# Kernel tuning notes

Measured on AMD Instinct MI355X. Metric: run time of the kernel, lower is better.

Reference implementation:

```python
import jax, jax.numpy as jnp
import numpy as np

S, N, H, E, L = 2048, 32, 512, 256, 2


def setup_inputs() -> dict:
    key = jax.random.key(0)
    ks = jax.random.split(key, 16)
    s = 0.05  # weight scale for stability
    return {
        "x": jax.random.randint(ks[0], (N,), 0, 10),
        "encoder_states": jax.random.normal(ks[1], (S, N, 2 * H), jnp.float32),
        "hidden": jax.random.normal(ks[2], (L, N, H), jnp.float32),
        "cell": jax.random.normal(ks[3], (L, N, H), jnp.float32),
        "W_energy": jax.random.normal(ks[4], (1, 3 * H), jnp.float32) * s,
        "b_energy": jnp.zeros((1,), jnp.float32),
        "emb_table": jax.random.normal(ks[5], (10, E), jnp.float32),
        "wih0": jax.random.normal(ks[6], (4 * H, 2 * H + E), jnp.float32) * s,
        "whh0": jax.random.normal(ks[7], (4 * H, H), jnp.float32) * s,
        "bih0": jnp.zeros((4 * H,), jnp.float32),
        "bhh0": jnp.zeros((4 * H,), jnp.float32),
        "wih1": jax.random.normal(ks[8], (4 * H, H), jnp.float32) * s,
        "whh1": jax.random.normal(ks[9], (4 * H, H), jnp.float32) * s,
        "bih1": jnp.zeros((4 * H,), jnp.float32),
        "bhh1": jnp.zeros((4 * H,), jnp.float32),
        "Wc": jax.random.normal(ks[10], (10, H), jnp.float32) * s,
        "bc": jnp.zeros((10,), jnp.float32),
    }


def _lstm_cell(x, h, c, wih, whh, bih, bhh):
    # PyTorch gate order: i, f, g, o
    gates = x @ wih.T + bih + h @ whh.T + bhh  # [N, 4H]
    i, f, g, o = jnp.split(gates, 4, axis=-1)
    c_new = jax.nn.sigmoid(f) * c + jax.nn.sigmoid(i) * jnp.tanh(g)
    h_new = jax.nn.sigmoid(o) * jnp.tanh(c_new)
    return h_new, c_new


def reference(x, encoder_states, hidden, cell, W_energy, b_energy, emb_table,
              wih0, whh0, bih0, bhh0, wih1, whh1, bih1, bhh1, Wc, bc):
    seq_len = encoder_states.shape[0]
    h_last = hidden[-1]  # [N, H]
    h_rep = jnp.broadcast_to(h_last, (seq_len,) + h_last.shape)  # [S, N, H]
    cat = jnp.concatenate([h_rep, encoder_states], axis=2)  # [S, N, 3H]
    energy = jax.nn.relu(cat @ W_energy.T + b_energy)  # [S, N, 1]
    attn = jax.nn.softmax(energy, axis=0)  # softmax over seq dim
    context = jnp.einsum('snk,snl->knl', attn, encoder_states)  # [1, N, 2H]
    emb = emb_table[x][None]  # [1, N, E]
    inp = jnp.concatenate([context, emb], axis=2)[0]  # [N, 2H+E]
    h0, c0 = _lstm_cell(inp, hidden[0], cell[0], wih0, whh0, bih0, bhh0)
    h1, c1 = _lstm_cell(h0, hidden[1], cell[1], wih1, whh1, bih1, bhh1)
    predictions = h1 @ Wc.T + bc  # [N, 10]
    hidden_new = jnp.stack([h0, h1], axis=0)
    cell_new = jnp.stack([c0, c1], axis=0)
    return predictions, hidden_new, cell_new
```

## Files before the change

### kernel.cpp

```cpp
#include <hip/hip_runtime.h>

#define SS 2048
#define NN_ 32
#define HH 512
#define EE 256
#define TWO_H 1024

#define OUT_PRED 0
#define OUT_H0 320
#define OUT_H1 16704
#define OUT_C0 33088
#define OUT_C1 49472

#define WS_ACC 0
#define WS_SUMW 1048576
#define WS_XCAT0 1049600
#define WS_PG0 0
#define WS_XCAT1 262144
#define WS_PG1 294912

__device__ __forceinline__ float wave_reduce(float v) {
  v += __shfl_xor(v, 32);
  v += __shfl_xor(v, 16);
  v += __shfl_xor(v, 8);
  v += __shfl_xor(v, 4);
  v += __shfl_xor(v, 2);
  v += __shfl_xor(v, 1);
  return v;
}

__device__ __forceinline__ float sigmoidf_(float x) { return 1.0f / (1.0f + __expf(-x)); }

__global__ __launch_bounds__(256, 4) void attn_pass(
    const float* __restrict__ enc, const float* __restrict__ hidden,
    const float* __restrict__ We, const float* __restrict__ be,
    float* __restrict__ ws) {
  const int blk = blockIdx.x;
  const int n = blk >> 5;
  const int chunk = blk & 31;
  const int t = threadIdx.x;
  const int wave = t >> 6;
  const int lane = t & 63;

  const float* hl = hidden + (size_t)(NN_ + n) * HH;
  float cp;
  {
    float4 a = *(const float4*)(hl + lane * 8);
    float4 b = *(const float4*)(hl + lane * 8 + 4);
    float4 wa = *(const float4*)(We + lane * 8);
    float4 wb = *(const float4*)(We + lane * 8 + 4);
    cp = a.x * wa.x + a.y * wa.y + a.z * wa.z + a.w * wa.w +
         b.x * wb.x + b.y * wb.y + b.z * wb.z + b.w * wb.w;
  }
  cp = wave_reduce(cp);
  const float c_n = cp + be[0];

  const float4 w0 = *(const float4*)(We + HH + 0 * 256 + lane * 4);
  const float4 w1 = *(const float4*)(We + HH + 1 * 256 + lane * 4);
  const float4 w2 = *(const float4*)(We + HH + 2 * 256 + lane * 4);
  const float4 w3 = *(const float4*)(We + HH + 3 * 256 + lane * 4);

  float4 acc0 = {0, 0, 0, 0}, acc1 = {0, 0, 0, 0}, acc2 = {0, 0, 0, 0}, acc3 = {0, 0, 0, 0};
  float sumw = 0.f;

  const int sBase = chunk * 64 + wave * 16;
#pragma unroll 2
  for (int i = 0; i < 16; ++i) {
    const float* row = enc + ((size_t)(sBase + i) * NN_ + n) * TWO_H;
    float4 e0 = *(const float4*)(row + 0 * 256 + lane * 4);
    float4 e1 = *(const float4*)(row + 1 * 256 + lane * 4);
    float4 e2 = *(const float4*)(row + 2 * 256 + lane * 4);
    float4 e3 = *(const float4*)(row + 3 * 256 + lane * 4);
    float d = e0.x * w0.x + e0.y * w0.y + e0.z * w0.z + e0.w * w0.w +
              e1.x * w1.x + e1.y * w1.y + e1.z * w1.z + e1.w * w1.w +
              e2.x * w2.x + e2.y * w2.y + e2.z * w2.z + e2.w * w2.w +
              e3.x * w3.x + e3.y * w3.y + e3.z * w3.z + e3.w * w3.w;
    d = wave_reduce(d);
    float en = c_n + d;
    en = en > 0.f ? en : 0.f;
    float p = __expf(en - 4.0f);
    sumw += p;
    acc0.x = fmaf(p, e0.x, acc0.x); acc0.y = fmaf(p, e0.y, acc0.y);
    acc0.z = fmaf(p, e0.z, acc0.z); acc0.w = fmaf(p, e0.w, acc0.w);
    acc1.x = fmaf(p, e1.x, acc1.x); acc1.y = fmaf(p, e1.y, acc1.y);
    acc1.z = fmaf(p, e1.z, acc1.z); acc1.w = fmaf(p, e1.w, acc1.w);
    acc2.x = fmaf(p, e2.x, acc2.x); acc2.y = fmaf(p, e2.y, acc2.y);
    acc2.z = fmaf(p, e2.z, acc2.z); acc2.w = fmaf(p, e2.w, acc2.w);
    acc3.x = fmaf(p, e3.x, acc3.x); acc3.y = fmaf(p, e3.y, acc3.y);
    acc3.z = fmaf(p, e3.z, acc3.z); acc3.w = fmaf(p, e3.w, acc3.w);
  }

  __shared__ __align__(16) float lacc[4][1024];
  __shared__ float lsum[4];
  *(float4*)&lacc[wave][0 * 256 + lane * 4] = acc0;
  *(float4*)&lacc[wave][1 * 256 + lane * 4] = acc1;
  *(float4*)&lacc[wave][2 * 256 + lane * 4] = acc2;
  *(float4*)&lacc[wave][3 * 256 + lane * 4] = acc3;
  if (lane == 0) lsum[wave] = sumw;
  __syncthreads();

  const int j = t * 4;
  float4 o;
  o.x = lacc[0][j + 0] + lacc[1][j + 0] + lacc[2][j + 0] + lacc[3][j + 0];
  o.y = lacc[0][j + 1] + lacc[1][j + 1] + lacc[2][j + 1] + lacc[3][j + 1];
  o.z = lacc[0][j + 2] + lacc[1][j + 2] + lacc[2][j + 2] + lacc[3][j + 2];
  o.w = lacc[0][j + 3] + lacc[1][j + 3] + lacc[2][j + 3] + lacc[3][j + 3];
  *(float4*)&ws[WS_ACC + (size_t)blk * 1024 + j] = o;
  if (t == 0) ws[WS_SUMW + blk] = lsum[0] + lsum[1] + lsum[2] + lsum[3];
}

__global__ __launch_bounds__(256) void reduce_ctx(
    const int* __restrict__ x, const float* __restrict__ emb,
    const float* __restrict__ hidden, float* ws) {
  const int n = blockIdx.x;
  const int t = threadIdx.x;
  float sumw = 0.f;
#pragma unroll
  for (int c = 0; c < 32; ++c) sumw += ws[WS_SUMW + n * 32 + c];
  const float inv = 1.0f / sumw;
  float4 v = {0, 0, 0, 0};
#pragma unroll 4
  for (int c = 0; c < 32; ++c) {
    float4 a = *(const float4*)&ws[WS_ACC + (size_t)(n * 32 + c) * 1024 + t * 4];
    v.x += a.x; v.y += a.y; v.z += a.z; v.w += a.w;
  }
  const int j = t * 4;
  ws[WS_XCAT0 + (j + 0) * NN_ + n] = v.x * inv;
  ws[WS_XCAT0 + (j + 1) * NN_ + n] = v.y * inv;
  ws[WS_XCAT0 + (j + 2) * NN_ + n] = v.z * inv;
  ws[WS_XCAT0 + (j + 3) * NN_ + n] = v.w * inv;
  if (t < 64) {
    const int e0 = t * 4;
    const int xi = x[n];
#pragma unroll
    for (int q = 0; q < 4; ++q)
      ws[WS_XCAT0 + (1024 + e0 + q) * NN_ + n] = emb[xi * EE + e0 + q];
  }
  if (t < 128) {
    const int k0 = t * 4;
#pragma unroll
    for (int q = 0; q < 4; ++q)
      ws[WS_XCAT0 + (1280 + k0 + q) * NN_ + n] = hidden[(size_t)n * HH + k0 + q];
  }
}

__global__ __launch_bounds__(256) void gates0_kernel(
    const float* __restrict__ wih0, const float* __restrict__ whh0, float* __restrict__ ws) {
  __shared__ __align__(16) float xs[448 * 32];
  const int bid = blockIdx.x;
  const int chunk = bid & 3;
  const int hg = bid >> 2;
  const int t = threadIdx.x;
  const int nn = t & 31;
  const int rl = t >> 5;
  const int h = hg * 8 + rl;

  const int kb = chunk * 448;
  const int ke = kb + 448;

  const float* src = ws + WS_XCAT0 + (size_t)kb * 32;
  for (int i = t * 4; i < 448 * 32; i += 1024)
    *(float4*)&xs[i] = *(const float4*)&src[i];
  __syncthreads();

  float a0 = 0.f, a1 = 0.f, a2 = 0.f, a3 = 0.f;

  {
    const int s0e = ke < 1280 ? ke : 1280;
    if (kb < s0e) {
      const float* p0 = wih0 + (size_t)(0 * 512 + h) * 1280 + kb;
      const float* p1 = wih0 + (size_t)(1 * 512 + h) * 1280 + kb;
      const float* p2 = wih0 + (size_t)(2 * 512 + h) * 1280 + kb;
      const float* p3 = wih0 + (size_t)(3 * 512 + h) * 1280 + kb;
      const int len = s0e - kb;
#pragma unroll 2
      for (int k = 0; k < len; k += 4) {
        const float4 w0 = *(const float4*)(p0 + k);
        const float4 w1 = *(const float4*)(p1 + k);
        const float4 w2 = *(const float4*)(p2 + k);
        const float4 w3 = *(const float4*)(p3 + k);
        const float x0 = xs[(k + 0) * 32 + nn];
        const float x1 = xs[(k + 1) * 32 + nn];
        const float x2 = xs[(k + 2) * 32 + nn];
        const float x3 = xs[(k + 3) * 32 + nn];
        a0 += w0.x * x0 + w0.y * x1 + w0.z * x2 + w0.w * x3;
        a1 += w1.x * x0 + w1.y * x1 + w1.z * x2 + w1.w * x3;
        a2 += w2.x * x0 + w2.y * x1 + w2.z * x2 + w2.w * x3;
        a3 += w3.x * x0 + w3.y * x1 + w3.z * x2 + w3.w * x3;
      }
    }
  }
  {
    const int s1b = kb > 1280 ? kb : 1280;
    if (s1b < ke) {
      const int xoff = s1b - kb;
      const float* q0 = whh0 + (size_t)(0 * 512 + h) * 512 + (s1b - 1280);
      const float* q1 = whh0 + (size_t)(1 * 512 + h) * 512 + (s1b - 1280);
      const float* q2 = whh0 + (size_t)(2 * 512 + h) * 512 + (s1b - 1280);
      const float* q3 = whh0 + (size_t)(3 * 512 + h) * 512 + (s1b - 1280);
      const int len = ke - s1b;
#pragma unroll 2
      for (int k = 0; k < len; k += 4) {
        const float4 w0 = *(const float4*)(q0 + k);
        const float4 w1 = *(const float4*)(q1 + k);
        const float4 w2 = *(const float4*)(q2 + k);
        const float4 w3 = *(const float4*)(q3 + k);
        const float x0 = xs[(k + xoff + 0) * 32 + nn];
        const float x1 = xs[(k + xoff + 1) * 32 + nn];
        const float x2 = xs[(k + xoff + 2) * 32 + nn];
        const float x3 = xs[(k + xoff + 3) * 32 + nn];
        a0 += w0.x * x0 + w0.y * x1 + w0.z * x2 + w0.w * x3;
        a1 += w1.x * x0 + w1.y * x1 + w1.z * x2 + w1.w * x3;
        a2 += w2.x * x0 + w2.y * x1 + w2.z * x2 + w2.w * x3;
        a3 += w3.x * x0 + w3.y * x1 + w3.z * x2 + w3.w * x3;
      }
    }
  }

  float* dst = ws + WS_PG0 + ((size_t)chunk * 2048 + h) * 32 + nn;
  dst[0 * 512 * 32] = a0;
  dst[1 * 512 * 32] = a1;
  dst[2 * 512 * 32] = a2;
  dst[3 * 512 * 32] = a3;
}

__global__ __launch_bounds__(256) void lstm0_kernel(
    const float* __restrict__ cell, const float* __restrict__ hidden,
    const float* __restrict__ bih0, const float* __restrict__ bhh0,
    float* __restrict__ out, float* __restrict__ ws) {
  const int g = blockIdx.x * 256 + threadIdx.x;
  const int nn = g & 31;
  const int h = g >> 5;
  float gi = bih0[h] + bhh0[h];
  float gf = bih0[512 + h] + bhh0[512 + h];
  float gg = bih0[1024 + h] + bhh0[1024 + h];
  float go = bih0[1536 + h] + bhh0[1536 + h];
#pragma unroll
  for (int c = 0; c < 4; ++c) {
    const float* p = ws + WS_PG0 + (size_t)c * 2048 * 32;
    gi += p[(0 * 512 + h) * 32 + nn];
    gf += p[(1 * 512 + h) * 32 + nn];
    gg += p[(2 * 512 + h) * 32 + nn];
    go += p[(3 * 512 + h) * 32 + nn];
  }
  const float cprev = cell[(size_t)nn * HH + h];
  const float c0 = sigmoidf_(gf) * cprev + sigmoidf_(gi) * tanhf(gg);
  const float h0 = sigmoidf_(go) * tanhf(c0);
  out[OUT_H0 + nn * HH + h] = h0;
  out[OUT_C0 + nn * HH + h] = c0;
  ws[WS_XCAT1 + h * 32 + nn] = h0;
  ws[WS_XCAT1 + (512 + h) * 32 + nn] = hidden[(size_t)(NN_ + nn) * HH + h];
}

__global__ __launch_bounds__(256) void gates1_kernel(
    const float* __restrict__ wih1, const float* __restrict__ whh1, float* __restrict__ ws) {
  __shared__ __align__(16) float xs[256 * 32];
  const int bid = blockIdx.x;
  const int chunk = bid & 3;
  const int hg = bid >> 2;
  const int t = threadIdx.x;
  const int nn = t & 31;
  const int rl = t >> 5;
  const int h = hg * 8 + rl;
  const int kb = chunk * 256;

  const float* src = ws + WS_XCAT1 + (size_t)kb * 32;
  for (int i = t * 4; i < 256 * 32; i += 1024)
    *(float4*)&xs[i] = *(const float4*)&src[i];
  __syncthreads();

  const float* base = (chunk < 2) ? wih1 : whh1;
  const int koff = (chunk < 2) ? kb : kb - 512;
  const float* p0 = base + (size_t)(0 * 512 + h) * 512 + koff;
  const float* p1 = base + (size_t)(1 * 512 + h) * 512 + koff;
  const float* p2 = base + (size_t)(2 * 512 + h) * 512 + koff;
  const float* p3 = base + (size_t)(3 * 512 + h) * 512 + koff;

  float a0 = 0.f, a1 = 0.f, a2 = 0.f, a3 = 0.f;
#pragma unroll 2
  for (int k = 0; k < 256; k += 4) {
    const float4 w0 = *(const float4*)(p0 + k);
    const float4 w1 = *(const float4*)(p1 + k);
    const float4 w2 = *(const float4*)(p2 + k);
    const float4 w3 = *(const float4*)(p3 + k);
    const float x0 = xs[(k + 0) * 32 + nn];
    const float x1 = xs[(k + 1) * 32 + nn];
    const float x2 = xs[(k + 2) * 32 + nn];
    const float x3 = xs[(k + 3) * 32 + nn];
    a0 += w0.x * x0 + w0.y * x1 + w0.z * x2 + w0.w * x3;
    a1 += w1.x * x0 + w1.y * x1 + w1.z * x2 + w1.w * x3;
    a2 += w2.x * x0 + w2.y * x1 + w2.z * x2 + w2.w * x3;
    a3 += w3.x * x0 + w3.y * x1 + w3.z * x2 + w3.w * x3;
  }

  float* dst = ws + WS_PG1 + ((size_t)chunk * 2048 + h) * 32 + nn;
  dst[0 * 512 * 32] = a0;
  dst[1 * 512 * 32] = a1;
  dst[2 * 512 * 32] = a2;
  dst[3 * 512 * 32] = a3;
}

__global__ __launch_bounds__(256) void lstm1_kernel(
    const float* __restrict__ cell,
    const float* __restrict__ bih1, const float* __restrict__ bhh1,
    float* __restrict__ out, float* __restrict__ ws) {
  const int g = blockIdx.x * 256 + threadIdx.x;
  const int nn = g & 31;
  const int h = g >> 5;
  float gi = bih1[h] + bhh1[h];
  float gf = bih1[512 + h] + bhh1[512 + h];
  float gg = bih1[1024 + h] + bhh1[1024 + h];
  float go = bih1[1536 + h] + bhh1[1536 + h];
#pragma unroll
  for (int c = 0; c < 4; ++c) {
    const float* p = ws + WS_PG1 + (size_t)c * 2048 * 32;
    gi += p[(0 * 512 + h) * 32 + nn];
    gf += p[(1 * 512 + h) * 32 + nn];
    gg += p[(2 * 512 + h) * 32 + nn];
    go += p[(3 * 512 + h) * 32 + nn];
  }
  const float cprev = cell[(size_t)(NN_ + nn) * HH + h];
  const float c1 = sigmoidf_(gf) * cprev + sigmoidf_(gi) * tanhf(gg);
  const float h1 = sigmoidf_(go) * tanhf(c1);
  out[OUT_H1 + nn * HH + h] = h1;
  out[OUT_C1 + nn * HH + h] = c1;
}

__global__ __launch_bounds__(256) void pred_kernel(
    const float* __restrict__ Wc, const float* __restrict__ bc, float* out) {
  const int wid = blockIdx.x * 4 + (threadIdx.x >> 6);
  const int lane = threadIdx.x & 63;
  const int nn = wid / 10;
  const int c = wid % 10;
  const float* hp = out + OUT_H1 + (size_t)nn * HH;
  const float* wp = Wc + (size_t)c * HH;
  float p = 0.f;
#pragma unroll
  for (int j = 0; j < 8; ++j) p += hp[lane * 8 + j] * wp[lane * 8 + j];
  p = wave_reduce(p);
  if (lane == 0) out[OUT_PRED + nn * 10 + c] = p + bc[c];
}

extern "C" void kernel_launch(void* const* d_in, const int* in_sizes, int n_in,
                              void* d_out, int out_size, void* d_ws, size_t ws_size,
                              hipStream_t stream) {
  const int* x = (const int*)d_in[0];
  const float* enc = (const float*)d_in[1];
  const float* hidden = (const float*)d_in[2];
  const float* cell = (const float*)d_in[3];
  const float* We = (const float*)d_in[4];
  const float* be = (const float*)d_in[5];
  const float* emb = (const float*)d_in[6];
  const float* wih0 = (const float*)d_in[7];
  const float* whh0 = (const float*)d_in[8];
  const float* bih0 = (const float*)d_in[9];
  const float* bhh0 = (const float*)d_in[10];
  const float* wih1 = (const float*)d_in[11];
  const float* whh1 = (const float*)d_in[12];
  const float* bih1 = (const float*)d_in[13];
  const float* bhh1 = (const float*)d_in[14];
  const float* Wc = (const float*)d_in[15];
  const float* bc = (const float*)d_in[16];
  float* out = (float*)d_out;
  float* ws = (float*)d_ws;

  hipLaunchKernelGGL(attn_pass, dim3(1024), dim3(256), 0, stream, enc, hidden, We, be, ws);
  hipLaunchKernelGGL(reduce_ctx, dim3(32), dim3(256), 0, stream, x, emb, hidden, ws);
  hipLaunchKernelGGL(gates0_kernel, dim3(256), dim3(256), 0, stream, wih0, whh0, ws);
  hipLaunchKernelGGL(lstm0_kernel, dim3(64), dim3(256), 0, stream, cell, hidden, bih0, bhh0, out, ws);
  hipLaunchKernelGGL(gates1_kernel, dim3(256), dim3(256), 0, stream, wih1, whh1, ws);
  hipLaunchKernelGGL(lstm1_kernel, dim3(64), dim3(256), 0, stream, cell, bih1, bhh1, out, ws);
  hipLaunchKernelGGL(pred_kernel, dim3(80), dim3(256), 0, stream, Wc, bc, out);
}
```

Baseline: 98.12 us.

## Stage LSTM gate weights in shared memory and split K across more blocks

The gate GEMV kernels now load each block's weight tile into padded shared memory with coalesced float4 loads, replacing the strided per-thread global reads. K is split into more chunks (7 for layer 0, 8 for layer 1), so more blocks run, and the LSTM epilogues sum more partials. reduce_ctx is also spread over 256 blocks so the context reduction uses more parallelism. This costs more shared memory per block, more partial-sum traffic, and workspace offsets moved to fit the larger partial buffers.

```diff
diff --git a/kernel.cpp b/kernel.cpp
--- a/kernel.cpp
+++ b/kernel.cpp
@@ -16,8 +16,8 @@
 #define WS_SUMW 1048576
 #define WS_XCAT0 1049600
 #define WS_PG0 0
-#define WS_XCAT1 262144
-#define WS_PG1 294912
+#define WS_XCAT1 458752
+#define WS_PG1 491520
 
 __device__ __forceinline__ float wave_reduce(float v) {
   v += __shfl_xor(v, 32);
@@ -111,112 +111,87 @@
 
 __global__ __launch_bounds__(256) void reduce_ctx(
     const int* __restrict__ x, const float* __restrict__ emb,
-    const float* __restrict__ hidden, float* ws) {
-  const int n = blockIdx.x;
+    const float* __restrict__ hidden, float* __restrict__ ws) {
+  const int b = blockIdx.x;
+  const int n = b >> 3;
+  const int jg = b & 7;
   const int t = threadIdx.x;
-  float sumw = 0.f;
-#pragma unroll
-  for (int c = 0; c < 32; ++c) sumw += ws[WS_SUMW + n * 32 + c];
-  const float inv = 1.0f / sumw;
-  float4 v = {0, 0, 0, 0};
-#pragma unroll 4
-  for (int c = 0; c < 32; ++c) {
-    float4 a = *(const float4*)&ws[WS_ACC + (size_t)(n * 32 + c) * 1024 + t * 4];
-    v.x += a.x; v.y += a.y; v.z += a.z; v.w += a.w;
-  }
-  const int j = t * 4;
-  ws[WS_XCAT0 + (j + 0) * NN_ + n] = v.x * inv;
-  ws[WS_XCAT0 + (j + 1) * NN_ + n] = v.y * inv;
-  ws[WS_XCAT0 + (j + 2) * NN_ + n] = v.z * inv;
-  ws[WS_XCAT0 + (j + 3) * NN_ + n] = v.w * inv;
-  if (t < 64) {
-    const int e0 = t * 4;
-    const int xi = x[n];
-#pragma unroll
-    for (int q = 0; q < 4; ++q)
-      ws[WS_XCAT0 + (1024 + e0 + q) * NN_ + n] = emb[xi * EE + e0 + q];
-  }
   if (t < 128) {
-    const int k0 = t * 4;
-#pragma unroll
-    for (int q = 0; q < 4; ++q)
-      ws[WS_XCAT0 + (1280 + k0 + q) * NN_ + n] = hidden[(size_t)n * HH + k0 + q];
-  }
-}
-
-__global__ __launch_bounds__(256) void gates0_kernel(
+    const int j = jg * 128 + t;
+    float sumw = 0.f;
+#pragma unroll
+    for (int c = 0; c < 32; ++c) sumw += ws[WS_SUMW + n * 32 + c];
+    const float inv = 1.0f / sumw;
+    float v = 0.f;
+#pragma unroll 8
+    for (int c = 0; c < 32; ++c) v += ws[WS_ACC + (size_t)(n * 32 + c) * 1024 + j];
+    ws[WS_XCAT0 + j * NN_ + n] = v * inv;
+  } else if (t < 224) {
+    const int row = jg * 96 + (t - 128);
+    float v;
+    if (row < 256) {
+      v = emb[(size_t)x[n] * EE + row];
+    } else {
+      v = hidden[(size_t)n * HH + (row - 256)];
+    }
+    ws[WS_XCAT0 + (1024 + row) * NN_ + n] = v;
+  }
+}
+
+__global__ __launch_bounds__(256, 2) void gates0_kernel(
     const float* __restrict__ wih0, const float* __restrict__ whh0, float* __restrict__ ws) {
-  __shared__ __align__(16) float xs[448 * 32];
+  __shared__ __align__(16) float xs[256 * 32];
+  __shared__ __align__(16) float wt[32 * 260];
   const int bid = blockIdx.x;
-  const int chunk = bid & 3;
-  const int hg = bid >> 2;
+  const int chunk = bid % 7;
+  const int hg = bid / 7;
   const int t = threadIdx.x;
   const int nn = t & 31;
   const int rl = t >> 5;
+
+  {
+    const float* src = ws + WS_XCAT0 + (size_t)chunk * 256 * 32;
+#pragma unroll
+    for (int i = t * 4; i < 8192; i += 1024)
+      *(float4*)&xs[i] = *(const float4*)&src[i];
+  }
+  {
+    const int r = t >> 3;
+    const int k8 = t & 7;
+    const int grow = (r >> 3) * 512 + hg * 8 + (r & 7);
+    const float* src = (chunk < 5) ? (wih0 + (size_t)grow * 1280 + chunk * 256)
+                                   : (whh0 + (size_t)grow * 512 + (chunk - 5) * 256);
+#pragma unroll
+    for (int jj = 0; jj < 8; ++jj) {
+      const int kl = jj * 32 + k8 * 4;
+      *(float4*)&wt[r * 260 + kl] = *(const float4*)(src + kl);
+    }
+  }
+  __syncthreads();
+
+  const float* w0p = &wt[(0 * 8 + rl) * 260];
+  const float* w1p = &wt[(1 * 8 + rl) * 260];
+  const float* w2p = &wt[(2 * 8 + rl) * 260];
+  const float* w3p = &wt[(3 * 8 + rl) * 260];
+
+  float a0 = 0.f, a1 = 0.f, a2 = 0.f, a3 = 0.f;
+#pragma unroll 4
+  for (int k = 0; k < 256; k += 4) {
+    const float4 w0 = *(const float4*)(w0p + k);
+    const float4 w1 = *(const float4*)(w1p + k);
+    const float4 w2 = *(const float4*)(w2p + k);
+    const float4 w3 = *(const float4*)(w3p + k);
+    const float x0 = xs[(k + 0) * 32 + nn];
+    const float x1 = xs[(k + 1) * 32 + nn];
+    const float x2 = xs[(k + 2) * 32 + nn];
+    const float x3 = xs[(k + 3) * 32 + nn];
+    a0 += w0.x * x0 + w0.y * x1 + w0.z * x2 + w0.w * x3;
+    a1 += w1.x * x0 + w1.y * x1 + w1.z * x2 + w1.w * x3;
+    a2 += w2.x * x0 + w2.y * x1 + w2.z * x2 + w2.w * x3;
+    a3 += w3.x * x0 + w3.y * x1 + w3.z * x2 + w3.w * x3;
+  }
+
   const int h = hg * 8 + rl;
-
-  const int kb = chunk * 448;
-  const int ke = kb + 448;
-
-  const float* src = ws + WS_XCAT0 + (size_t)kb * 32;
-  for (int i = t * 4; i < 448 * 32; i += 1024)
-    *(float4*)&xs[i] = *(const float4*)&src[i];
-  __syncthreads();
-
-  float a0 = 0.f, a1 = 0.f, a2 = 0.f, a3 = 0.f;
-
-  {
-    const int s0e = ke < 1280 ? ke : 1280;
-    if (kb < s0e) {
-      const float* p0 = wih0 + (size_t)(0 * 512 + h) * 1280 + kb;
-      const float* p1 = wih0 + (size_t)(1 * 512 + h) * 1280 + kb;
-      const float* p2 = wih0 + (size_t)(2 * 512 + h) * 1280 + kb;
-      const float* p3 = wih0 + (size_t)(3 * 512 + h) * 1280 + kb;
-      const int len = s0e - kb;
-#pragma unroll 2
-      for (int k = 0; k < len; k += 4) {
-        const float4 w0 = *(const float4*)(p0 + k);
-        const float4 w1 = *(const float4*)(p1 + k);
-        const float4 w2 = *(const float4*)(p2 + k);
-        const float4 w3 = *(const float4*)(p3 + k);
-        const float x0 = xs[(k + 0) * 32 + nn];
-        const float x1 = xs[(k + 1) * 32 + nn];
-        const float x2 = xs[(k + 2) * 32 + nn];
-        const float x3 = xs[(k + 3) * 32 + nn];
-        a0 += w0.x * x0 + w0.y * x1 + w0.z * x2 + w0.w * x3;
-        a1 += w1.x * x0 + w1.y * x1 + w1.z * x2 + w1.w * x3;
-        a2 += w2.x * x0 + w2.y * x1 + w2.z * x2 + w2.w * x3;
-        a3 += w3.x * x0 + w3.y * x1 + w3.z * x2 + w3.w * x3;
-      }
-    }
-  }
-  {
-    const int s1b = kb > 1280 ? kb : 1280;
-    if (s1b < ke) {
-      const int xoff = s1b - kb;
-      const float* q0 = whh0 + (size_t)(0 * 512 + h) * 512 + (s1b - 1280);
-      const float* q1 = whh0 + (size_t)(1 * 512 + h) * 512 + (s1b - 1280);
-      const float* q2 = whh0 + (size_t)(2 * 512 + h) * 512 + (s1b - 1280);
-      const float* q3 = whh0 + (size_t)(3 * 512 + h) * 512 + (s1b - 1280);
-      const int len = ke - s1b;
-#pragma unroll 2
-      for (int k = 0; k < len; k += 4) {
-        const float4 w0 = *(const float4*)(q0 + k);
-        const float4 w1 = *(const float4*)(q1 + k);
-        const float4 w2 = *(const float4*)(q2 + k);
-        const float4 w3 = *(const float4*)(q3 + k);
-        const float x0 = xs[(k + xoff + 0) * 32 + nn];
-        const float x1 = xs[(k + xoff + 1) * 32 + nn];
-        const float x2 = xs[(k + xoff + 2) * 32 + nn];
-        const float x3 = xs[(k + xoff + 3) * 32 + nn];
-        a0 += w0.x * x0 + w0.y * x1 + w0.z * x2 + w0.w * x3;
-        a1 += w1.x * x0 + w1.y * x1 + w1.z * x2 + w1.w * x3;
-        a2 += w2.x * x0 + w2.y * x1 + w2.z * x2 + w2.w * x3;
-        a3 += w3.x * x0 + w3.y * x1 + w3.z * x2 + w3.w * x3;
-      }
-    }
-  }
-
   float* dst = ws + WS_PG0 + ((size_t)chunk * 2048 + h) * 32 + nn;
   dst[0 * 512 * 32] = a0;
   dst[1 * 512 * 32] = a1;
@@ -236,7 +211,7 @@
   float gg = bih0[1024 + h] + bhh0[1024 + h];
   float go = bih0[1536 + h] + bhh0[1536 + h];
 #pragma unroll
-  for (int c = 0; c < 4; ++c) {
+  for (int c = 0; c < 7; ++c) {
     const float* p = ws + WS_PG0 + (size_t)c * 2048 * 32;
     gi += p[(0 * 512 + h) * 32 + nn];
     gf += p[(1 * 512 + h) * 32 + nn];
@@ -252,37 +227,50 @@
   ws[WS_XCAT1 + (512 + h) * 32 + nn] = hidden[(size_t)(NN_ + nn) * HH + h];
 }
 
-__global__ __launch_bounds__(256) void gates1_kernel(
+__global__ __launch_bounds__(256, 2) void gates1_kernel(
     const float* __restrict__ wih1, const float* __restrict__ whh1, float* __restrict__ ws) {
-  __shared__ __align__(16) float xs[256 * 32];
+  __shared__ __align__(16) float xs[128 * 32];
+  __shared__ __align__(16) float wt[32 * 132];
   const int bid = blockIdx.x;
-  const int chunk = bid & 3;
-  const int hg = bid >> 2;
+  const int chunk = bid & 7;
+  const int hg = bid >> 3;
   const int t = threadIdx.x;
   const int nn = t & 31;
   const int rl = t >> 5;
-  const int h = hg * 8 + rl;
-  const int kb = chunk * 256;
-
-  const float* src = ws + WS_XCAT1 + (size_t)kb * 32;
-  for (int i = t * 4; i < 256 * 32; i += 1024)
-    *(float4*)&xs[i] = *(const float4*)&src[i];
+  const int kb = chunk * 128;
+
+  {
+    const float* src = ws + WS_XCAT1 + (size_t)kb * 32;
+#pragma unroll
+    for (int i = t * 4; i < 4096; i += 1024)
+      *(float4*)&xs[i] = *(const float4*)&src[i];
+  }
+  {
+    const int r = t >> 3;
+    const int k8 = t & 7;
+    const int grow = (r >> 3) * 512 + hg * 8 + (r & 7);
+    const float* src = (chunk < 4) ? (wih1 + (size_t)grow * 512 + kb)
+                                   : (whh1 + (size_t)grow * 512 + (kb - 512));
+#pragma unroll
+    for (int jj = 0; jj < 4; ++jj) {
+      const int kl = jj * 32 + k8 * 4;
+      *(float4*)&wt[r * 132 + kl] = *(const float4*)(src + kl);
+    }
+  }
   __syncthreads();
 
-  const float* base = (chunk < 2) ? wih1 : whh1;
-  const int koff = (chunk < 2) ? kb : kb - 512;
-  const float* p0 = base + (size_t)(0 * 512 + h) * 512 + koff;
-  const float* p1 = base + (size_t)(1 * 512 + h) * 512 + koff;
-  const float* p2 = base + (size_t)(2 * 512 + h) * 512 + koff;
-  const float* p3 = base + (size_t)(3 * 512 + h) * 512 + koff;
+  const float* w0p = &wt[(0 * 8 + rl) * 132];
+  const float* w1p = &wt[(1 * 8 + rl) * 132];
+  const float* w2p = &wt[(2 * 8 + rl) * 132];
+  const float* w3p = &wt[(3 * 8 + rl) * 132];
 
   float a0 = 0.f, a1 = 0.f, a2 = 0.f, a3 = 0.f;
-#pragma unroll 2
-  for (int k = 0; k < 256; k += 4) {
-    const float4 w0 = *(const float4*)(p0 + k);
-    const float4 w1 = *(const float4*)(p1 + k);
-    const float4 w2 = *(const float4*)(p2 + k);
-    const float4 w3 = *(const float4*)(p3 + k);
+#pragma unroll 4
+  for (int k = 0; k < 128; k += 4) {
+    const float4 w0 = *(const float4*)(w0p + k);
+    const float4 w1 = *(const float4*)(w1p + k);
+    const float4 w2 = *(const float4*)(w2p + k);
+    const float4 w3 = *(const float4*)(w3p + k);
     const float x0 = xs[(k + 0) * 32 + nn];
     const float x1 = xs[(k + 1) * 32 + nn];
     const float x2 = xs[(k + 2) * 32 + nn];
@@ -293,6 +281,7 @@
     a3 += w3.x * x0 + w3.y * x1 + w3.z * x2 + w3.w * x3;
   }
 
+  const int h = hg * 8 + rl;
   float* dst = ws + WS_PG1 + ((size_t)chunk * 2048 + h) * 32 + nn;
   dst[0 * 512 * 32] = a0;
   dst[1 * 512 * 32] = a1;
@@ -312,7 +301,7 @@
   float gg = bih1[1024 + h] + bhh1[1024 + h];
   float go = bih1[1536 + h] + bhh1[1536 + h];
 #pragma unroll
-  for (int c = 0; c < 4; ++c) {
+  for (int c = 0; c < 8; ++c) {
     const float* p = ws + WS_PG1 + (size_t)c * 2048 * 32;
     gi += p[(0 * 512 + h) * 32 + nn];
     gf += p[(1 * 512 + h) * 32 + nn];
@@ -365,10 +354,10 @@
   float* ws = (float*)d_ws;
 
   hipLaunchKernelGGL(attn_pass, dim3(1024), dim3(256), 0, stream, enc, hidden, We, be, ws);
-  hipLaunchKernelGGL(reduce_ctx, dim3(32), dim3(256), 0, stream, x, emb, hidden, ws);
-  hipLaunchKernelGGL(gates0_kernel, dim3(256), dim3(256), 0, stream, wih0, whh0, ws);
+  hipLaunchKernelGGL(reduce_ctx, dim3(256), dim3(256), 0, stream, x, emb, hidden, ws);
+  hipLaunchKernelGGL(gates0_kernel, dim3(448), dim3(256), 0, stream, wih0, whh0, ws);
   hipLaunchKernelGGL(lstm0_kernel, dim3(64), dim3(256), 0, stream, cell, hidden, bih0, bhh0, out, ws);
-  hipLaunchKernelGGL(gates1_kernel, dim3(256), dim3(256), 0, stream, wih1, whh1, ws);
+  hipLaunchKernelGGL(gates1_kernel, dim3(512), dim3(256), 0, stream, wih1, whh1, ws);
   hipLaunchKernelGGL(lstm1_kernel, dim3(64), dim3(256), 0, stream, cell, bih1, bhh1, out, ws);
   hipLaunchKernelGGL(pred_kernel, dim3(80), dim3(256), 0, stream, Wc, bc, out);
 }
```

Measured after the change: 78.94 us. 1.24x faster.
